# Performance work log

Hardware: AMD Instinct MI355X
Metric: run time of the kernel (lower is better)

## Reference

```python
import jax, jax.numpy as jnp
import numpy as np

N = 50000          # num nodes
E = 600000         # num edges
F_IN = 128         # num_features
H = 128            # graph_hidden_dim
R = 2              # num_relations
L = 3              # n_layers_conv
BN_EPS = 1e-5
BN_BETA = 1e-4     # BatchNorm bias init per module code


def setup_inputs() -> dict:
    key = jax.random.key(0)
    ks = jax.random.split(key, 9)
    s_in = 1.0 / np.sqrt(F_IN)
    s_h = 1.0 / np.sqrt(H)
    return {
        "x": jax.random.normal(ks[0], (N, F_IN), jnp.float32),
        "edge_index": jax.random.randint(ks[1], (2, E), 0, N, jnp.int32),
        "edge_type": jax.random.randint(ks[2], (E,), 0, R, jnp.int32),
        "W0_rel": jax.random.normal(ks[3], (R, F_IN, H), jnp.float32) * s_in,
        "W0_root": jax.random.normal(ks[4], (F_IN, H), jnp.float32) * s_in,
        "b0": jnp.zeros((H,), jnp.float32),
        "Ws_rel": jax.random.normal(ks[5], (L, R, H, H), jnp.float32) * s_h,
        "Ws_root": jax.random.normal(ks[6], (L, H, H), jnp.float32) * s_h,
        "bs": jnp.zeros((L, H), jnp.float32),
    }


def batchnorm(x):
    # training-mode BatchNorm1d over nodes; weight=1, bias=1e-4 (per init)
    mu = jnp.mean(x, axis=0)
    var = jnp.mean((x - mu) ** 2, axis=0)  # biased var, as torch uses for norm
    return (x - mu) * jax.lax.rsqrt(var + BN_EPS) + BN_BETA


def rgcn_conv(x, src, dst, edge_type, W_rel, W_root, b):
    # PyG RGCNConv, aggr='mean': per-relation mean of x[src] at dst,
    # then per-relation linear, plus root transform and bias.
    seg = dst * R + edge_type  # combined (node, relation) segment id
    msgs = x[src]                                   # [E, d] gather
    sums = jax.ops.segment_sum(msgs, seg, num_segments=N * R)
    cnts = jax.ops.segment_sum(jnp.ones((src.shape[0],), x.dtype), seg,
                               num_segments=N * R)
    mean = sums.reshape(N, R, -1) / jnp.maximum(cnts, 1.0).reshape(N, R, 1)
    out = jnp.einsum('nrd,rdh->nh', mean, W_rel) + x @ W_root + b
    return out


def reference(x, edge_index, edge_type, W0_rel, W0_root, b0, Ws_rel, Ws_root, bs):
    src, dst = edge_index[0], edge_index[1]
    h = batchnorm(x)
    h = jax.nn.relu(rgcn_conv(h, src, dst, edge_type, W0_rel, W0_root, b0))
    for i in range(L):
        h_ = batchnorm(h)
        h_ = jax.nn.relu(rgcn_conv(h_, src, dst, edge_type,
                                   Ws_rel[i], Ws_root[i], bs[i]))
        h = h + h_  # conv_residual=True
    return h  # gconv_dropout == 0
```

## Files before the change

kernel.cpp:

```cpp
#include <hip/hip_runtime.h>
#include <hip/hip_bf16.h>

#define N_NODES 50000
#define N_EDGES 600000
#define F 128
#define R 2
#define NLAYER 4
#define NSEG (N_NODES * R)
#define NSCB 98
#define NB 384
#define BN_EPS 1e-5f
#define BETA 1e-4f

typedef __hip_bfloat16 bf16;
typedef __attribute__((ext_vector_type(8))) short short8;
typedef __attribute__((ext_vector_type(4))) float floatx4;

__global__ void k_wt(const float* __restrict__ W0_rel, const float* __restrict__ W0_root,
                     const float* __restrict__ Ws_rel, const float* __restrict__ Ws_root,
                     bf16* __restrict__ Bt) {
    int idx = blockIdx.x * 256 + threadIdx.x;
    if (idx >= NLAYER * NB * F) return;
    int l = idx / (NB * F);
    int rem = idx % (NB * F);
    int j = rem / F, d = rem % F;
    float v;
    if (j < 256) {
        int r = j >> 7, c = j & 127;
        v = (l == 0) ? W0_rel[(r * F + d) * F + c]
                     : Ws_rel[((size_t)((l - 1) * R + r) * F + d) * F + c];
    } else {
        int c = j - 256;
        v = (l == 0) ? W0_root[d * F + c]
                     : Ws_root[((size_t)(l - 1) * F + d) * F + c];
    }
    Bt[idx] = __float2bfloat16(v);
}

__global__ void k_count(const int* __restrict__ dst, const int* __restrict__ et,
                        int* __restrict__ cnt) {
    int e = blockIdx.x * 256 + threadIdx.x;
    if (e < N_EDGES) atomicAdd(&cnt[dst[e] * R + et[e]], 1);
}

__global__ void k_scan1(const int* __restrict__ cnt, int* __restrict__ off,
                        int* __restrict__ bsum) {
    int t = threadIdx.x;
    int g = blockIdx.x * 1024 + t;
    int v = (g < NSEG) ? cnt[g] : 0;
    int lane = t & 63;
    int wv = t >> 6;
    int x = v;
    for (int d = 1; d < 64; d <<= 1) {
        int y = __shfl_up(x, d, 64);
        if (lane >= d) x += y;
    }
    __shared__ int wtot[16];
    if (lane == 63) wtot[wv] = x;
    __syncthreads();
    if (t < 16) {
        int s = wtot[t];
        for (int d = 1; d < 16; d <<= 1) {
            int y = __shfl_up(s, d, 64);
            if (t >= d) s += y;
        }
        wtot[t] = s;
    }
    __syncthreads();
    int wpre = (wv == 0) ? 0 : wtot[wv - 1];
    int incl = x + wpre;
    if (g < NSEG) off[g] = incl - v;
    if (t == 1023) bsum[blockIdx.x] = incl;
}

__global__ void k_scan2(int* __restrict__ bsum) {
    __shared__ int s[128];
    int t = threadIdx.x;
    int v = (t < NSCB) ? bsum[t] : 0;
    s[t] = v;
    __syncthreads();
    for (int d = 1; d < 128; d <<= 1) {
        int y = (t >= d) ? s[t - d] : 0;
        __syncthreads();
        s[t] += y;
        __syncthreads();
    }
    if (t < NSCB) bsum[t] = s[t] - v;
}

__global__ void k_scan3(int* __restrict__ off, const int* __restrict__ bsum) {
    int g = blockIdx.x * 1024 + threadIdx.x;
    if (g < NSEG) off[g] += bsum[blockIdx.x];
}

__global__ void k_fill(const int* __restrict__ src, const int* __restrict__ dst,
                       const int* __restrict__ et, const int* __restrict__ off,
                       int* __restrict__ fill, int* __restrict__ esrc) {
    int e = blockIdx.x * 256 + threadIdx.x;
    if (e >= N_EDGES) return;
    int seg = dst[e] * R + et[e];
    int idx = off[seg] + atomicAdd(&fill[seg], 1);
    esrc[idx] = src[e];
}

__global__ void k_bnstats(const float* __restrict__ h, float* __restrict__ gs) {
    int c = threadIdx.x & 127;
    int rl = threadIdx.x >> 7;
    float s = 0.f, q = 0.f;
    for (int r = blockIdx.x * 2 + rl; r < N_NODES; r += gridDim.x * 2) {
        float v = h[(size_t)r * F + c];
        s += v; q += v * v;
    }
    __shared__ float ls[256], lq[256];
    ls[threadIdx.x] = s; lq[threadIdx.x] = q;
    __syncthreads();
    if (rl == 0) {
        atomicAdd(&gs[c], ls[c] + ls[c + 128]);
        atomicAdd(&gs[128 + c], lq[c] + lq[c + 128]);
    }
}

__launch_bounds__(512)
__global__ void k_gemm(const float* __restrict__ h, const float* __restrict__ gs,
                       const bf16* __restrict__ Bt, const float* __restrict__ bias,
                       bf16* __restrict__ y, float* __restrict__ z) {
    __shared__ bf16 As[64 * 136];
    __shared__ bf16 Bs[128 * 136];
    int t = threadIdx.x;
    int m0 = blockIdx.x * 64;
    int c4 = (t & 31) * 4;
    float mu[4], rs[4];
    for (int c = 0; c < 4; c++) {
        float mm = gs[c4 + c] * (1.0f / N_NODES);
        float qq = gs[128 + c4 + c] * (1.0f / N_NODES);
        mu[c] = mm;
        rs[c] = rsqrtf(qq - mm * mm + BN_EPS);
    }
    int r0 = t >> 5;
    for (int it = 0; it < 4; it++) {
        int row = r0 + it * 16;
        int m = m0 + row;
        float4 v = {0.f, 0.f, 0.f, 0.f};
        if (m < N_NODES) v = *(const float4*)(h + (size_t)m * F + c4);
        bf16 o[4];
        o[0] = __float2bfloat16((v.x - mu[0]) * rs[0] + BETA);
        o[1] = __float2bfloat16((v.y - mu[1]) * rs[1] + BETA);
        o[2] = __float2bfloat16((v.z - mu[2]) * rs[2] + BETA);
        o[3] = __float2bfloat16((v.w - mu[3]) * rs[3] + BETA);
        *(double*)(As + row * 136 + c4) = *(const double*)o;
    }
    __syncthreads();
    int w = t >> 6;
    int lane = t & 63;
    int msub = w & 3;
    int nh = w >> 2;
    int lm = lane & 15;
    int lq = lane >> 4;
    short8 a[4];
    for (int ki = 0; ki < 4; ki++)
        a[ki] = *(const short8*)(As + (msub * 16 + lm) * 136 + ki * 32 + lq * 8);
    int m = m0 + msub * 16 + lm;
    for (int ci = 0; ci < 3; ci++) {
        __syncthreads();
        {
            const bf16* bsrc = Bt + (size_t)ci * 128 * F;
            for (int rr = 0; rr < 4; rr++) {
                int idx = rr * 512 + t;
                int row = idx >> 4;
                int kc = idx & 15;
                short8 v = *(const short8*)(bsrc + row * F + kc * 8);
                *(short8*)(Bs + row * 136 + kc * 8) = v;
            }
        }
        __syncthreads();
        for (int tt = 0; tt < 4; tt++) {
            int nt = nh * 4 + tt;
            short8 b[4];
            for (int ki = 0; ki < 4; ki++)
                b[ki] = *(const short8*)(Bs + (nt * 16 + lm) * 136 + ki * 32 + lq * 8);
            floatx4 acc = {0.f, 0.f, 0.f, 0.f};
            for (int ki = 0; ki < 4; ki++)
                acc = __builtin_amdgcn_mfma_f32_16x16x32_bf16(b[ki], a[ki], acc, 0, 0, 0);
            int n0 = ci * 128 + nt * 16 + lq * 4;
            if (m < N_NODES) {
                if (ci < 2) {
                    union { bf16 o[4]; double d; } u;
                    u.o[0] = __float2bfloat16(acc[0]);
                    u.o[1] = __float2bfloat16(acc[1]);
                    u.o[2] = __float2bfloat16(acc[2]);
                    u.o[3] = __float2bfloat16(acc[3]);
                    *(double*)(y + (size_t)m * 256 + n0) = u.d;
                } else {
                    float4 bv = *(const float4*)(bias + (n0 - 256));
                    float4 o4;
                    o4.x = acc[0] + bv.x;
                    o4.y = acc[1] + bv.y;
                    o4.z = acc[2] + bv.z;
                    o4.w = acc[3] + bv.w;
                    *(float4*)(z + (size_t)m * F + (n0 - 256)) = o4;
                }
            }
        }
    }
}

__global__ void k_aggregate(const bf16* __restrict__ y, const float* __restrict__ z,
                            const int* __restrict__ cnt, const int* __restrict__ off,
                            const int* __restrict__ esrc,
                            float* __restrict__ h, float* __restrict__ outp, int layer) {
    int wid = (blockIdx.x * 256 + threadIdx.x) >> 6;
    int lane = threadIdx.x & 63;
    if (wid >= N_NODES) return;
    int n = wid;
    int f = lane * 2;
    int2 cc = *(const int2*)(cnt + n * R);
    int c0 = cc.x, c1 = cc.y;
    int o0 = off[n * R];
    int ctot = c0 + c1;
    float inv0 = (c0 > 0) ? 1.0f / (float)c0 : 0.f;
    float inv1 = (c1 > 0) ? 1.0f / (float)c1 : 0.f;
    const bf16* yb = y + f;
    float2 zz = *(const float2*)(z + (size_t)n * F + f);
    float2 hp; hp.x = 0.f; hp.y = 0.f;
    if (layer > 0) hp = *(const float2*)(h + (size_t)n * F + f);
    float sa[8], sb[8];
    #pragma unroll
    for (int k = 0; k < 8; k++) { sa[k] = 0.f; sb[k] = 0.f; }
    int i = 0;
    for (; i + 8 <= ctot; i += 8) {
        int sn[8];
        #pragma unroll
        for (int k = 0; k < 8; k++) sn[k] = esrc[o0 + i + k];
        __hip_bfloat162 p[8];
        #pragma unroll
        for (int k = 0; k < 8; k++) {
            int ro = (i + k >= c0) ? 128 : 0;
            p[k] = *(const __hip_bfloat162*)(yb + (size_t)sn[k] * 256 + ro);
        }
        #pragma unroll
        for (int k = 0; k < 8; k++) {
            float wk = (i + k >= c0) ? inv1 : inv0;
            sa[k] = fmaf(__bfloat162float(p[k].x), wk, sa[k]);
            sb[k] = fmaf(__bfloat162float(p[k].y), wk, sb[k]);
        }
    }
    if (i + 4 <= ctot) {
        int sn[4];
        #pragma unroll
        for (int k = 0; k < 4; k++) sn[k] = esrc[o0 + i + k];
        __hip_bfloat162 p[4];
        #pragma unroll
        for (int k = 0; k < 4; k++) {
            int ro = (i + k >= c0) ? 128 : 0;
            p[k] = *(const __hip_bfloat162*)(yb + (size_t)sn[k] * 256 + ro);
        }
        #pragma unroll
        for (int k = 0; k < 4; k++) {
            float wk = (i + k >= c0) ? inv1 : inv0;
            sa[k] = fmaf(__bfloat162float(p[k].x), wk, sa[k]);
            sb[k] = fmaf(__bfloat162float(p[k].y), wk, sb[k]);
        }
        i += 4;
    }
    for (; i < ctot; i++) {
        int sn = esrc[o0 + i];
        int ro = (i >= c0) ? 128 : 0;
        float wk = (i >= c0) ? inv1 : inv0;
        __hip_bfloat162 p = *(const __hip_bfloat162*)(yb + (size_t)sn * 256 + ro);
        sa[0] = fmaf(__bfloat162float(p.x), wk, sa[0]);
        sb[0] = fmaf(__bfloat162float(p.y), wk, sb[0]);
    }
    float a0 = zz.x + (((sa[0] + sa[1]) + (sa[2] + sa[3])) + ((sa[4] + sa[5]) + (sa[6] + sa[7])));
    float a1 = zz.y + (((sb[0] + sb[1]) + (sb[2] + sb[3])) + ((sb[4] + sb[5]) + (sb[6] + sb[7])));
    a0 = fmaxf(a0, 0.f);
    a1 = fmaxf(a1, 0.f);
    a0 += hp.x;
    a1 += hp.y;
    float2 o2; o2.x = a0; o2.y = a1;
    *(float2*)(h + (size_t)n * F + f) = o2;
    if (outp) {
        float2 q2; q2.x = a0; q2.y = a1;
        *(float2*)(outp + (size_t)n * F + f) = q2;
    }
}

extern "C" void kernel_launch(void* const* d_in, const int* in_sizes, int n_in,
                              void* d_out, int out_size, void* d_ws, size_t ws_size,
                              hipStream_t stream) {
    const float* x       = (const float*)d_in[0];
    const int*   eidx    = (const int*)d_in[1];
    const int*   etype   = (const int*)d_in[2];
    const float* W0_rel  = (const float*)d_in[3];
    const float* W0_root = (const float*)d_in[4];
    const float* b0      = (const float*)d_in[5];
    const float* Ws_rel  = (const float*)d_in[6];
    const float* Ws_root = (const float*)d_in[7];
    const float* bs      = (const float*)d_in[8];
    const int* src = eidx;
    const int* dst = eidx + N_EDGES;

    char* w = (char*)d_ws;
    float* h   = (float*)w; w += (size_t)N_NODES * F * 4;
    float* z   = (float*)w; w += (size_t)N_NODES * F * 4;
    bf16*  y   = (bf16*)w;  w += (size_t)N_NODES * 256 * 2;
    bf16*  Bt  = (bf16*)w;  w += (size_t)NLAYER * NB * F * 2;
    int* cnt   = (int*)w;   w += (size_t)NSEG * 4;
    int* fill  = (int*)w;   w += (size_t)NSEG * 4;
    float* stats = (float*)w; w += (size_t)NLAYER * 256 * 4;
    int* off   = (int*)w;   w += (size_t)NSEG * 4;
    int* esrc  = (int*)w;   w += (size_t)N_EDGES * 4;
    int* bsum  = (int*)w;   w += 128 * 4;

    hipMemsetAsync(cnt, 0, (size_t)NSEG * 4 * 2 + (size_t)NLAYER * 256 * 4, stream);
    k_wt<<<(NLAYER * NB * F + 255) / 256, 256, 0, stream>>>(W0_rel, W0_root, Ws_rel, Ws_root, Bt);
    k_count<<<(N_EDGES + 255) / 256, 256, 0, stream>>>(dst, etype, cnt);
    k_scan1<<<NSCB, 1024, 0, stream>>>(cnt, off, bsum);
    k_scan2<<<1, 128, 0, stream>>>(bsum);
    k_scan3<<<NSCB, 1024, 0, stream>>>(off, bsum);
    k_fill<<<(N_EDGES + 255) / 256, 256, 0, stream>>>(src, dst, etype, off, fill, esrc);

    for (int l = 0; l < NLAYER; l++) {
        float* gs = stats + l * 256;
        const float* bias = (l == 0) ? b0 : (bs + (size_t)(l - 1) * F);
        const float* hin = (l == 0) ? x : h;
        k_bnstats<<<512, 256, 0, stream>>>(hin, gs);
        k_gemm<<<(N_NODES + 63) / 64, 512, 0, stream>>>(
            hin, gs, Bt + (size_t)l * NB * F, bias, y, z);
        k_aggregate<<<(N_NODES * 64 + 255) / 256, 256, 0, stream>>>(
            y, z, cnt, off, esrc, h, (l == 3) ? (float*)d_out : nullptr, l);
    }
}
```

Measured before the change: 487.3 us.

## Reorder RGCN layer to aggregate normalized features before the fused GEMM

Each layer now follows a new order. A standalone kernel writes the batch-normalized input as a bf16 N×128 array. A gather kernel computes per-relation mean messages from that array into an N×256 buffer. A single K=384 MFMA GEMM then applies the relation and root weights, with bias, ReLU and the residual fused into its epilogue. The goal is to gather from a compact 128-wide bf16 table instead of a 256-wide transformed one, improving cache locality, and to accumulate the whole output in registers within one GEMM. The cost is an extra elementwise kernel, an extra intermediate write and read per layer, and an unguarded tail-block read past the last node row.

```diff
diff --git a/kernel.cpp b/kernel.cpp
--- a/kernel.cpp
+++ b/kernel.cpp
@@ -8,7 +8,7 @@
 #define NLAYER 4
 #define NSEG (N_NODES * R)
 #define NSCB 98
-#define NB 384
+#define KTOT 384
 #define BN_EPS 1e-5f
 #define BETA 1e-4f
 
@@ -18,23 +18,23 @@
 
 __global__ void k_wt(const float* __restrict__ W0_rel, const float* __restrict__ W0_root,
                      const float* __restrict__ Ws_rel, const float* __restrict__ Ws_root,
-                     bf16* __restrict__ Bt) {
+                     bf16* __restrict__ Bt2) {
     int idx = blockIdx.x * 256 + threadIdx.x;
-    if (idx >= NLAYER * NB * F) return;
-    int l = idx / (NB * F);
-    int rem = idx % (NB * F);
-    int j = rem / F, d = rem % F;
+    if (idx >= NLAYER * F * KTOT) return;
+    int l = idx / (F * KTOT);
+    int rem = idx % (F * KTOT);
+    int j = rem / KTOT, k = rem % KTOT;
     float v;
-    if (j < 256) {
-        int r = j >> 7, c = j & 127;
-        v = (l == 0) ? W0_rel[(r * F + d) * F + c]
-                     : Ws_rel[((size_t)((l - 1) * R + r) * F + d) * F + c];
+    if (k < 256) {
+        int r = k >> 7, d = k & 127;
+        v = (l == 0) ? W0_rel[((size_t)r * F + d) * F + j]
+                     : Ws_rel[((size_t)((l - 1) * R + r) * F + d) * F + j];
     } else {
-        int c = j - 256;
-        v = (l == 0) ? W0_root[d * F + c]
-                     : Ws_root[((size_t)(l - 1) * F + d) * F + c];
-    }
-    Bt[idx] = __float2bfloat16(v);
+        int d = k - 256;
+        v = (l == 0) ? W0_root[(size_t)d * F + j]
+                     : Ws_root[((size_t)(l - 1) * F + d) * F + j];
+    }
+    Bt2[idx] = __float2bfloat16(v);
 }
 
 __global__ void k_count(const int* __restrict__ dst, const int* __restrict__ et,
@@ -120,94 +120,54 @@
     }
 }
 
-__launch_bounds__(512)
-__global__ void k_gemm(const float* __restrict__ h, const float* __restrict__ gs,
-                       const bf16* __restrict__ Bt, const float* __restrict__ bias,
-                       bf16* __restrict__ y, float* __restrict__ z) {
-    __shared__ bf16 As[64 * 136];
-    __shared__ bf16 Bs[128 * 136];
-    int t = threadIdx.x;
-    int m0 = blockIdx.x * 64;
-    int c4 = (t & 31) * 4;
-    float mu[4], rs[4];
+__global__ void k_bn(const float* __restrict__ hin, const float* __restrict__ gs,
+                     bf16* __restrict__ hbn) {
+    int idx = blockIdx.x * 256 + threadIdx.x;
+    if (idx >= N_NODES * F / 4) return;
+    int c4 = (idx * 4) & 127;
+    float4 v = *(const float4*)(hin + (size_t)idx * 4);
+    bf16 o[4];
+    float vv[4] = {v.x, v.y, v.z, v.w};
+    #pragma unroll
     for (int c = 0; c < 4; c++) {
         float mm = gs[c4 + c] * (1.0f / N_NODES);
         float qq = gs[128 + c4 + c] * (1.0f / N_NODES);
-        mu[c] = mm;
-        rs[c] = rsqrtf(qq - mm * mm + BN_EPS);
-    }
-    int r0 = t >> 5;
-    for (int it = 0; it < 4; it++) {
-        int row = r0 + it * 16;
-        int m = m0 + row;
-        float4 v = {0.f, 0.f, 0.f, 0.f};
-        if (m < N_NODES) v = *(const float4*)(h + (size_t)m * F + c4);
-        bf16 o[4];
-        o[0] = __float2bfloat16((v.x - mu[0]) * rs[0] + BETA);
-        o[1] = __float2bfloat16((v.y - mu[1]) * rs[1] + BETA);
-        o[2] = __float2bfloat16((v.z - mu[2]) * rs[2] + BETA);
-        o[3] = __float2bfloat16((v.w - mu[3]) * rs[3] + BETA);
-        *(double*)(As + row * 136 + c4) = *(const double*)o;
-    }
-    __syncthreads();
-    int w = t >> 6;
-    int lane = t & 63;
-    int msub = w & 3;
-    int nh = w >> 2;
-    int lm = lane & 15;
-    int lq = lane >> 4;
-    short8 a[4];
-    for (int ki = 0; ki < 4; ki++)
-        a[ki] = *(const short8*)(As + (msub * 16 + lm) * 136 + ki * 32 + lq * 8);
-    int m = m0 + msub * 16 + lm;
-    for (int ci = 0; ci < 3; ci++) {
-        __syncthreads();
-        {
-            const bf16* bsrc = Bt + (size_t)ci * 128 * F;
-            for (int rr = 0; rr < 4; rr++) {
-                int idx = rr * 512 + t;
-                int row = idx >> 4;
-                int kc = idx & 15;
-                short8 v = *(const short8*)(bsrc + row * F + kc * 8);
-                *(short8*)(Bs + row * 136 + kc * 8) = v;
-            }
-        }
-        __syncthreads();
-        for (int tt = 0; tt < 4; tt++) {
-            int nt = nh * 4 + tt;
-            short8 b[4];
-            for (int ki = 0; ki < 4; ki++)
-                b[ki] = *(const short8*)(Bs + (nt * 16 + lm) * 136 + ki * 32 + lq * 8);
-            floatx4 acc = {0.f, 0.f, 0.f, 0.f};
-            for (int ki = 0; ki < 4; ki++)
-                acc = __builtin_amdgcn_mfma_f32_16x16x32_bf16(b[ki], a[ki], acc, 0, 0, 0);
-            int n0 = ci * 128 + nt * 16 + lq * 4;
-            if (m < N_NODES) {
-                if (ci < 2) {
-                    union { bf16 o[4]; double d; } u;
-                    u.o[0] = __float2bfloat16(acc[0]);
-                    u.o[1] = __float2bfloat16(acc[1]);
-                    u.o[2] = __float2bfloat16(acc[2]);
-                    u.o[3] = __float2bfloat16(acc[3]);
-                    *(double*)(y + (size_t)m * 256 + n0) = u.d;
-                } else {
-                    float4 bv = *(const float4*)(bias + (n0 - 256));
-                    float4 o4;
-                    o4.x = acc[0] + bv.x;
-                    o4.y = acc[1] + bv.y;
-                    o4.z = acc[2] + bv.z;
-                    o4.w = acc[3] + bv.w;
-                    *(float4*)(z + (size_t)m * F + (n0 - 256)) = o4;
-                }
-            }
-        }
-    }
-}
-
-__global__ void k_aggregate(const bf16* __restrict__ y, const float* __restrict__ z,
-                            const int* __restrict__ cnt, const int* __restrict__ off,
-                            const int* __restrict__ esrc,
-                            float* __restrict__ h, float* __restrict__ outp, int layer) {
+        float rs = rsqrtf(qq - mm * mm + BN_EPS);
+        o[c] = __float2bfloat16((vv[c] - mm) * rs + BETA);
+    }
+    *(double*)(hbn + (size_t)idx * 4) = *(const double*)o;
+}
+
+__device__ __forceinline__ void seg_sum(const bf16* __restrict__ hb,
+                                        const int* __restrict__ esrc,
+                                        int o, int c, float& rx, float& ry) {
+    float a0 = 0.f, a1 = 0.f, b0 = 0.f, b1 = 0.f;
+    float e0 = 0.f, e1 = 0.f, d0 = 0.f, d1 = 0.f;
+    int i = 0;
+    for (; i + 4 <= c; i += 4) {
+        int s0 = esrc[o + i], s1 = esrc[o + i + 1];
+        int s2 = esrc[o + i + 2], s3 = esrc[o + i + 3];
+        __hip_bfloat162 p0 = *(const __hip_bfloat162*)(hb + (size_t)s0 * F);
+        __hip_bfloat162 p1 = *(const __hip_bfloat162*)(hb + (size_t)s1 * F);
+        __hip_bfloat162 p2 = *(const __hip_bfloat162*)(hb + (size_t)s2 * F);
+        __hip_bfloat162 p3 = *(const __hip_bfloat162*)(hb + (size_t)s3 * F);
+        a0 += __bfloat162float(p0.x); a1 += __bfloat162float(p0.y);
+        b0 += __bfloat162float(p1.x); b1 += __bfloat162float(p1.y);
+        e0 += __bfloat162float(p2.x); e1 += __bfloat162float(p2.y);
+        d0 += __bfloat162float(p3.x); d1 += __bfloat162float(p3.y);
+    }
+    for (; i < c; i++) {
+        int sn = esrc[o + i];
+        __hip_bfloat162 p = *(const __hip_bfloat162*)(hb + (size_t)sn * F);
+        a0 += __bfloat162float(p.x); a1 += __bfloat162float(p.y);
+    }
+    rx = (a0 + b0) + (e0 + d0);
+    ry = (a1 + b1) + (e1 + d1);
+}
+
+__global__ void k_agg(const bf16* __restrict__ hbn,
+                      const int* __restrict__ cnt, const int* __restrict__ off,
+                      const int* __restrict__ esrc, bf16* __restrict__ mm) {
     int wid = (blockIdx.x * 256 + threadIdx.x) >> 6;
     int lane = threadIdx.x & 63;
     if (wid >= N_NODES) return;
@@ -216,71 +176,93 @@
     int2 cc = *(const int2*)(cnt + n * R);
     int c0 = cc.x, c1 = cc.y;
     int o0 = off[n * R];
-    int ctot = c0 + c1;
     float inv0 = (c0 > 0) ? 1.0f / (float)c0 : 0.f;
     float inv1 = (c1 > 0) ? 1.0f / (float)c1 : 0.f;
-    const bf16* yb = y + f;
-    float2 zz = *(const float2*)(z + (size_t)n * F + f);
-    float2 hp; hp.x = 0.f; hp.y = 0.f;
-    if (layer > 0) hp = *(const float2*)(h + (size_t)n * F + f);
-    float sa[8], sb[8];
+    const bf16* hb = hbn + f;
+    float s0x, s0y, s1x, s1y;
+    seg_sum(hb, esrc, o0, c0, s0x, s0y);
+    seg_sum(hb, esrc, o0 + c0, c1, s1x, s1y);
+    __hip_bfloat162 w0, w1;
+    w0.x = __float2bfloat16(s0x * inv0);
+    w0.y = __float2bfloat16(s0y * inv0);
+    w1.x = __float2bfloat16(s1x * inv1);
+    w1.y = __float2bfloat16(s1y * inv1);
+    *(__hip_bfloat162*)(mm + (size_t)n * 256 + f) = w0;
+    *(__hip_bfloat162*)(mm + (size_t)n * 256 + 128 + f) = w1;
+}
+
+__launch_bounds__(512)
+__global__ void k_gemm2(const bf16* __restrict__ mm, const bf16* __restrict__ hbn,
+                        const bf16* __restrict__ Bt2, const float* __restrict__ bias,
+                        float* __restrict__ h, float* __restrict__ outp, int layer) {
+    __shared__ bf16 As[64 * 136];
+    __shared__ bf16 Bs[128 * 136];
+    int t = threadIdx.x;
+    int m0 = blockIdx.x * 64;
+    int w = t >> 6;
+    int lane = t & 63;
+    int msub = w & 3;
+    int nh = w >> 2;
+    int lm = lane & 15;
+    int lq = lane >> 4;
+    int m = m0 + msub * 16 + lm;
+    floatx4 acc[4];
     #pragma unroll
-    for (int k = 0; k < 8; k++) { sa[k] = 0.f; sb[k] = 0.f; }
-    int i = 0;
-    for (; i + 8 <= ctot; i += 8) {
-        int sn[8];
+    for (int j = 0; j < 4; j++) acc[j] = (floatx4){0.f, 0.f, 0.f, 0.f};
+    for (int ci = 0; ci < 3; ci++) {
+        __syncthreads();
+        {
+            for (int rr = 0; rr < 2; rr++) {
+                int idx = rr * 512 + t;
+                int row = idx >> 4;
+                int kc = idx & 15;
+                const bf16* srcp = (ci < 2)
+                    ? (mm + (size_t)(m0 + row) * 256 + ci * 128 + kc * 8)
+                    : (hbn + (size_t)(m0 + row) * F + kc * 8);
+                *(short8*)(As + row * 136 + kc * 8) = *(const short8*)srcp;
+            }
+        }
+        {
+            for (int rr = 0; rr < 4; rr++) {
+                int idx = rr * 512 + t;
+                int row = idx >> 4;
+                int kc = idx & 15;
+                short8 v = *(const short8*)(Bt2 + (size_t)row * KTOT + ci * 128 + kc * 8);
+                *(short8*)(Bs + row * 136 + kc * 8) = v;
+            }
+        }
+        __syncthreads();
+        short8 a[4];
         #pragma unroll
-        for (int k = 0; k < 8; k++) sn[k] = esrc[o0 + i + k];
-        __hip_bfloat162 p[8];
+        for (int ki = 0; ki < 4; ki++)
+            a[ki] = *(const short8*)(As + (msub * 16 + lm) * 136 + ki * 32 + lq * 8);
+        for (int tt = 0; tt < 4; tt++) {
+            int nt = nh * 4 + tt;
+            short8 b[4];
+            #pragma unroll
+            for (int ki = 0; ki < 4; ki++)
+                b[ki] = *(const short8*)(Bs + (nt * 16 + lm) * 136 + ki * 32 + lq * 8);
+            #pragma unroll
+            for (int ki = 0; ki < 4; ki++)
+                acc[tt] = __builtin_amdgcn_mfma_f32_16x16x32_bf16(b[ki], a[ki], acc[tt], 0, 0, 0);
+        }
+    }
+    if (m < N_NODES) {
         #pragma unroll
-        for (int k = 0; k < 8; k++) {
-            int ro = (i + k >= c0) ? 128 : 0;
-            p[k] = *(const __hip_bfloat162*)(yb + (size_t)sn[k] * 256 + ro);
-        }
-        #pragma unroll
-        for (int k = 0; k < 8; k++) {
-            float wk = (i + k >= c0) ? inv1 : inv0;
-            sa[k] = fmaf(__bfloat162float(p[k].x), wk, sa[k]);
-            sb[k] = fmaf(__bfloat162float(p[k].y), wk, sb[k]);
-        }
-    }
-    if (i + 4 <= ctot) {
-        int sn[4];
-        #pragma unroll
-        for (int k = 0; k < 4; k++) sn[k] = esrc[o0 + i + k];
-        __hip_bfloat162 p[4];
-        #pragma unroll
-        for (int k = 0; k < 4; k++) {
-            int ro = (i + k >= c0) ? 128 : 0;
-            p[k] = *(const __hip_bfloat162*)(yb + (size_t)sn[k] * 256 + ro);
-        }
-        #pragma unroll
-        for (int k = 0; k < 4; k++) {
-            float wk = (i + k >= c0) ? inv1 : inv0;
-            sa[k] = fmaf(__bfloat162float(p[k].x), wk, sa[k]);
-            sb[k] = fmaf(__bfloat162float(p[k].y), wk, sb[k]);
-        }
-        i += 4;
-    }
-    for (; i < ctot; i++) {
-        int sn = esrc[o0 + i];
-        int ro = (i >= c0) ? 128 : 0;
-        float wk = (i >= c0) ? inv1 : inv0;
-        __hip_bfloat162 p = *(const __hip_bfloat162*)(yb + (size_t)sn * 256 + ro);
-        sa[0] = fmaf(__bfloat162float(p.x), wk, sa[0]);
-        sb[0] = fmaf(__bfloat162float(p.y), wk, sb[0]);
-    }
-    float a0 = zz.x + (((sa[0] + sa[1]) + (sa[2] + sa[3])) + ((sa[4] + sa[5]) + (sa[6] + sa[7])));
-    float a1 = zz.y + (((sb[0] + sb[1]) + (sb[2] + sb[3])) + ((sb[4] + sb[5]) + (sb[6] + sb[7])));
-    a0 = fmaxf(a0, 0.f);
-    a1 = fmaxf(a1, 0.f);
-    a0 += hp.x;
-    a1 += hp.y;
-    float2 o2; o2.x = a0; o2.y = a1;
-    *(float2*)(h + (size_t)n * F + f) = o2;
-    if (outp) {
-        float2 q2; q2.x = a0; q2.y = a1;
-        *(float2*)(outp + (size_t)n * F + f) = q2;
+        for (int tt = 0; tt < 4; tt++) {
+            int nt = nh * 4 + tt;
+            int n0 = nt * 16 + lq * 4;
+            float4 bv = *(const float4*)(bias + n0);
+            float4 hv = {0.f, 0.f, 0.f, 0.f};
+            if (layer > 0) hv = *(const float4*)(h + (size_t)m * F + n0);
+            float4 o4;
+            o4.x = fmaxf(acc[tt][0] + bv.x, 0.f) + hv.x;
+            o4.y = fmaxf(acc[tt][1] + bv.y, 0.f) + hv.y;
+            o4.z = fmaxf(acc[tt][2] + bv.z, 0.f) + hv.z;
+            o4.w = fmaxf(acc[tt][3] + bv.w, 0.f) + hv.w;
+            *(float4*)(h + (size_t)m * F + n0) = o4;
+            if (outp) *(float4*)(outp + (size_t)m * F + n0) = o4;
+        }
     }
 }
 
@@ -301,9 +283,9 @@
 
     char* w = (char*)d_ws;
     float* h   = (float*)w; w += (size_t)N_NODES * F * 4;
-    float* z   = (float*)w; w += (size_t)N_NODES * F * 4;
-    bf16*  y   = (bf16*)w;  w += (size_t)N_NODES * 256 * 2;
-    bf16*  Bt  = (bf16*)w;  w += (size_t)NLAYER * NB * F * 2;
+    bf16*  hbn = (bf16*)w;  w += (size_t)N_NODES * F * 2;
+    bf16*  mm  = (bf16*)w;  w += (size_t)N_NODES * 256 * 2;
+    bf16*  Bt2 = (bf16*)w;  w += (size_t)NLAYER * F * KTOT * 2;
     int* cnt   = (int*)w;   w += (size_t)NSEG * 4;
     int* fill  = (int*)w;   w += (size_t)NSEG * 4;
     float* stats = (float*)w; w += (size_t)NLAYER * 256 * 4;
@@ -312,7 +294,7 @@
     int* bsum  = (int*)w;   w += 128 * 4;
 
     hipMemsetAsync(cnt, 0, (size_t)NSEG * 4 * 2 + (size_t)NLAYER * 256 * 4, stream);
-    k_wt<<<(NLAYER * NB * F + 255) / 256, 256, 0, stream>>>(W0_rel, W0_root, Ws_rel, Ws_root, Bt);
+    k_wt<<<(NLAYER * F * KTOT + 255) / 256, 256, 0, stream>>>(W0_rel, W0_root, Ws_rel, Ws_root, Bt2);
     k_count<<<(N_EDGES + 255) / 256, 256, 0, stream>>>(dst, etype, cnt);
     k_scan1<<<NSCB, 1024, 0, stream>>>(cnt, off, bsum);
     k_scan2<<<1, 128, 0, stream>>>(bsum);
@@ -324,9 +306,10 @@
         const float* bias = (l == 0) ? b0 : (bs + (size_t)(l - 1) * F);
         const float* hin = (l == 0) ? x : h;
         k_bnstats<<<512, 256, 0, stream>>>(hin, gs);
-        k_gemm<<<(N_NODES + 63) / 64, 512, 0, stream>>>(
-            hin, gs, Bt + (size_t)l * NB * F, bias, y, z);
-        k_aggregate<<<(N_NODES * 64 + 255) / 256, 256, 0, stream>>>(
-            y, z, cnt, off, esrc, h, (l == 3) ? (float*)d_out : nullptr, l);
-    }
-}
+        k_bn<<<(N_NODES * F / 4 + 255) / 256, 256, 0, stream>>>(hin, gs, hbn);
+        k_agg<<<(N_NODES * 64 + 255) / 256, 256, 0, stream>>>(hbn, cnt, off, esrc, mm);
+        k_gemm2<<<(N_NODES + 63) / 64, 512, 0, stream>>>(
+            mm, hbn, Bt2 + (size_t)l * F * KTOT, bias, h,
+            (l == 3) ? (float*)d_out : nullptr, l);
+    }
+}
```

New measurement: 505.0 us. +3.6%, slower.

## Split aggregation per relation across wavefronts and store root output in bf16

Applied to the files above, without the earlier changes.

The aggregate kernel now gives each (node, relation) segment its own wavefront and combines the two relation partials through shared memory with a block barrier. This removes the per-edge relation select and weight multiply and doubles the parallelism for the edge gather, which is meant to cut latency on nodes with long edge lists. The root-transform output z is also stored as bf16 instead of fp32, halving its write and read traffic at some cost in precision. Index arithmetic in the weight-transpose kernel is widened to size_t as a minor cleanup.

```diff
diff --git a/kernel.cpp b/kernel.cpp
--- a/kernel.cpp
+++ b/kernel.cpp
@@ -27,11 +27,11 @@
     float v;
     if (j < 256) {
         int r = j >> 7, c = j & 127;
-        v = (l == 0) ? W0_rel[(r * F + d) * F + c]
+        v = (l == 0) ? W0_rel[((size_t)r * F + d) * F + c]
                      : Ws_rel[((size_t)((l - 1) * R + r) * F + d) * F + c];
     } else {
         int c = j - 256;
-        v = (l == 0) ? W0_root[d * F + c]
+        v = (l == 0) ? W0_root[(size_t)d * F + c]
                      : Ws_root[((size_t)(l - 1) * F + d) * F + c];
     }
     Bt[idx] = __float2bfloat16(v);
@@ -123,7 +123,7 @@
 __launch_bounds__(512)
 __global__ void k_gemm(const float* __restrict__ h, const float* __restrict__ gs,
                        const bf16* __restrict__ Bt, const float* __restrict__ bias,
-                       bf16* __restrict__ y, float* __restrict__ z) {
+                       bf16* __restrict__ y, bf16* __restrict__ z) {
     __shared__ bf16 As[64 * 136];
     __shared__ bf16 Bs[128 * 136];
     int t = threadIdx.x;
@@ -192,95 +192,97 @@
                     *(double*)(y + (size_t)m * 256 + n0) = u.d;
                 } else {
                     float4 bv = *(const float4*)(bias + (n0 - 256));
-                    float4 o4;
-                    o4.x = acc[0] + bv.x;
-                    o4.y = acc[1] + bv.y;
-                    o4.z = acc[2] + bv.z;
-                    o4.w = acc[3] + bv.w;
-                    *(float4*)(z + (size_t)m * F + (n0 - 256)) = o4;
+                    union { bf16 o[4]; double d; } u;
+                    u.o[0] = __float2bfloat16(acc[0] + bv.x);
+                    u.o[1] = __float2bfloat16(acc[1] + bv.y);
+                    u.o[2] = __float2bfloat16(acc[2] + bv.z);
+                    u.o[3] = __float2bfloat16(acc[3] + bv.w);
+                    *(double*)(z + (size_t)m * F + (n0 - 256)) = u.d;
                 }
             }
         }
     }
 }
 
-__global__ void k_aggregate(const bf16* __restrict__ y, const float* __restrict__ z,
+__global__ void k_aggregate(const bf16* __restrict__ y, const bf16* __restrict__ z,
                             const int* __restrict__ cnt, const int* __restrict__ off,
                             const int* __restrict__ esrc,
                             float* __restrict__ h, float* __restrict__ outp, int layer) {
-    int wid = (blockIdx.x * 256 + threadIdx.x) >> 6;
+    __shared__ float pa[4][64];
+    __shared__ float pb[4][64];
+    int wv = threadIdx.x >> 6;
     int lane = threadIdx.x & 63;
-    if (wid >= N_NODES) return;
-    int n = wid;
+    int wid2 = blockIdx.x * 4 + wv;
+    int n = wid2 >> 1;
+    int r = wid2 & 1;
     int f = lane * 2;
-    int2 cc = *(const int2*)(cnt + n * R);
-    int c0 = cc.x, c1 = cc.y;
-    int o0 = off[n * R];
-    int ctot = c0 + c1;
-    float inv0 = (c0 > 0) ? 1.0f / (float)c0 : 0.f;
-    float inv1 = (c1 > 0) ? 1.0f / (float)c1 : 0.f;
-    const bf16* yb = y + f;
-    float2 zz = *(const float2*)(z + (size_t)n * F + f);
-    float2 hp; hp.x = 0.f; hp.y = 0.f;
-    if (layer > 0) hp = *(const float2*)(h + (size_t)n * F + f);
+    int seg = n * R + r;
+    int c = cnt[seg];
+    int o = off[seg];
+    float inv = (c > 0) ? 1.0f / (float)c : 0.f;
+    const bf16* yb = y + (size_t)r * 128 + f;
     float sa[8], sb[8];
     #pragma unroll
     for (int k = 0; k < 8; k++) { sa[k] = 0.f; sb[k] = 0.f; }
     int i = 0;
-    for (; i + 8 <= ctot; i += 8) {
+    for (; i + 8 <= c; i += 8) {
         int sn[8];
         #pragma unroll
-        for (int k = 0; k < 8; k++) sn[k] = esrc[o0 + i + k];
+        for (int k = 0; k < 8; k++) sn[k] = esrc[o + i + k];
         __hip_bfloat162 p[8];
         #pragma unroll
+        for (int k = 0; k < 8; k++)
+            p[k] = *(const __hip_bfloat162*)(yb + (size_t)sn[k] * 256);
+        #pragma unroll
         for (int k = 0; k < 8; k++) {
-            int ro = (i + k >= c0) ? 128 : 0;
-            p[k] = *(const __hip_bfloat162*)(yb + (size_t)sn[k] * 256 + ro);
-        }
-        #pragma unroll
-        for (int k = 0; k < 8; k++) {
-            float wk = (i + k >= c0) ? inv1 : inv0;
-            sa[k] = fmaf(__bfloat162float(p[k].x), wk, sa[k]);
-            sb[k] = fmaf(__bfloat162float(p[k].y), wk, sb[k]);
-        }
-    }
-    if (i + 4 <= ctot) {
+            sa[k] += __bfloat162float(p[k].x);
+            sb[k] += __bfloat162float(p[k].y);
+        }
+    }
+    if (i + 4 <= c) {
         int sn[4];
         #pragma unroll
-        for (int k = 0; k < 4; k++) sn[k] = esrc[o0 + i + k];
+        for (int k = 0; k < 4; k++) sn[k] = esrc[o + i + k];
         __hip_bfloat162 p[4];
         #pragma unroll
+        for (int k = 0; k < 4; k++)
+            p[k] = *(const __hip_bfloat162*)(yb + (size_t)sn[k] * 256);
+        #pragma unroll
         for (int k = 0; k < 4; k++) {
-            int ro = (i + k >= c0) ? 128 : 0;
-            p[k] = *(const __hip_bfloat162*)(yb + (size_t)sn[k] * 256 + ro);
-        }
-        #pragma unroll
-        for (int k = 0; k < 4; k++) {
-            float wk = (i + k >= c0) ? inv1 : inv0;
-            sa[k] = fmaf(__bfloat162float(p[k].x), wk, sa[k]);
-            sb[k] = fmaf(__bfloat162float(p[k].y), wk, sb[k]);
+            sa[k] += __bfloat162float(p[k].x);
+            sb[k] += __bfloat162float(p[k].y);
         }
         i += 4;
     }
-    for (; i < ctot; i++) {
-        int sn = esrc[o0 + i];
-        int ro = (i >= c0) ? 128 : 0;
-        float wk = (i >= c0) ? inv1 : inv0;
-        __hip_bfloat162 p = *(const __hip_bfloat162*)(yb + (size_t)sn * 256 + ro);
-        sa[0] = fmaf(__bfloat162float(p.x), wk, sa[0]);
-        sb[0] = fmaf(__bfloat162float(p.y), wk, sb[0]);
-    }
-    float a0 = zz.x + (((sa[0] + sa[1]) + (sa[2] + sa[3])) + ((sa[4] + sa[5]) + (sa[6] + sa[7])));
-    float a1 = zz.y + (((sb[0] + sb[1]) + (sb[2] + sb[3])) + ((sb[4] + sb[5]) + (sb[6] + sb[7])));
-    a0 = fmaxf(a0, 0.f);
-    a1 = fmaxf(a1, 0.f);
-    a0 += hp.x;
-    a1 += hp.y;
-    float2 o2; o2.x = a0; o2.y = a1;
-    *(float2*)(h + (size_t)n * F + f) = o2;
-    if (outp) {
-        float2 q2; q2.x = a0; q2.y = a1;
-        *(float2*)(outp + (size_t)n * F + f) = q2;
+    for (; i < c; i++) {
+        int sn = esrc[o + i];
+        __hip_bfloat162 p = *(const __hip_bfloat162*)(yb + (size_t)sn * 256);
+        sa[0] += __bfloat162float(p.x);
+        sb[0] += __bfloat162float(p.y);
+    }
+    float px = (((sa[0] + sa[1]) + (sa[2] + sa[3])) + ((sa[4] + sa[5]) + (sa[6] + sa[7]))) * inv;
+    float py = (((sb[0] + sb[1]) + (sb[2] + sb[3])) + ((sb[4] + sb[5]) + (sb[6] + sb[7]))) * inv;
+    pa[wv][lane] = px;
+    pb[wv][lane] = py;
+    __syncthreads();
+    if ((wv & 1) == 0) {
+        float a0 = px + pa[wv + 1][lane];
+        float a1 = py + pb[wv + 1][lane];
+        __hip_bfloat162 zz = *(const __hip_bfloat162*)(z + (size_t)n * F + f);
+        a0 += __bfloat162float(zz.x);
+        a1 += __bfloat162float(zz.y);
+        a0 = fmaxf(a0, 0.f);
+        a1 = fmaxf(a1, 0.f);
+        if (layer > 0) {
+            float2 hp = *(const float2*)(h + (size_t)n * F + f);
+            a0 += hp.x; a1 += hp.y;
+        }
+        float2 o2; o2.x = a0; o2.y = a1;
+        *(float2*)(h + (size_t)n * F + f) = o2;
+        if (outp) {
+            float2 q2; q2.x = a0; q2.y = a1;
+            *(float2*)(outp + (size_t)n * F + f) = q2;
+        }
     }
 }
 
@@ -301,7 +303,7 @@
 
     char* w = (char*)d_ws;
     float* h   = (float*)w; w += (size_t)N_NODES * F * 4;
-    float* z   = (float*)w; w += (size_t)N_NODES * F * 4;
+    bf16*  z   = (bf16*)w;  w += (size_t)N_NODES * F * 2;
     bf16*  y   = (bf16*)w;  w += (size_t)N_NODES * 256 * 2;
     bf16*  Bt  = (bf16*)w;  w += (size_t)NLAYER * NB * F * 2;
     int* cnt   = (int*)w;   w += (size_t)NSEG * 4;
@@ -326,7 +328,7 @@
         k_bnstats<<<512, 256, 0, stream>>>(hin, gs);
         k_gemm<<<(N_NODES + 63) / 64, 512, 0, stream>>>(
             hin, gs, Bt + (size_t)l * NB * F, bias, y, z);
-        k_aggregate<<<(N_NODES * 64 + 255) / 256, 256, 0, stream>>>(
+        k_aggregate<<<NSEG / 4, 256, 0, stream>>>(
             y, z, cnt, off, esrc, h, (l == 3) ? (float*)d_out : nullptr, l);
     }
 }
```

Measured after the change: 536.5 us. 1.1x slower.
